# Kernel tuning notes

Hardware: AMD Instinct MI355X
Metric: run time of the kernel (lower is better)

## Reference

```python
import jax, jax.numpy as jnp
import numpy as np

FEATURE_DIM = 512


def setup_inputs() -> dict:
    key = jax.random.key(0)
    ks = jax.random.split(key, 12)
    B, Nv, Dv = 32, 1024, 768
    Nl, Dl = 77, 512
    D = FEATURE_DIM
    s = lambda fan_in: 1.0 / np.sqrt(fan_in)
    return {
        "fv": jax.random.normal(ks[0], (B, Nv, Dv), jnp.float32),
        "fl": jax.random.normal(ks[1], (B, Nl, Dl), jnp.float32),
        # linear_vk / linear_vv: Dv -> D (stored as [in, out])
        "W_vk": jax.random.uniform(ks[2], (Dv, D), jnp.float32, -s(Dv), s(Dv)),
        "b_vk": jax.random.uniform(ks[3], (D,), jnp.float32, -s(Dv), s(Dv)),
        "W_vv": jax.random.uniform(ks[4], (Dv, D), jnp.float32, -s(Dv), s(Dv)),
        "b_vv": jax.random.uniform(ks[5], (D,), jnp.float32, -s(Dv), s(Dv)),
        # linear_lk / linear_lv: Dl -> D
        "W_lk": jax.random.uniform(ks[6], (Dl, D), jnp.float32, -s(Dl), s(Dl)),
        "b_lk": jax.random.uniform(ks[7], (D,), jnp.float32, -s(Dl), s(Dl)),
        "W_lv": jax.random.uniform(ks[8], (Dl, D), jnp.float32, -s(Dl), s(Dl)),
        "b_lv": jax.random.uniform(ks[9], (D,), jnp.float32, -s(Dl), s(Dl)),
        # linear_m: nl(77) -> 768
        "W_m": jax.random.uniform(ks[10], (Nl, 768), jnp.float32, -s(Nl), s(Nl)),
        "b_m": jax.random.uniform(ks[11], (768,), jnp.float32, -s(Nl), s(Nl)),
    }


def reference(fv, fl, W_vk, b_vk, W_vv, b_vv, W_lk, b_lk, W_lv, b_lv, W_m, b_m):
    # projections
    fk_v = jnp.einsum("bvd,de->bve", fv, W_vk) + b_vk   # [B, Nv, D]
    fv_v = jnp.einsum("bvd,de->bve", fv, W_vv) + b_vv   # [B, Nv, D]
    fk_l = jnp.einsum("bld,de->ble", fl, W_lk) + b_lk   # [B, Nl, D]
    fv_l = jnp.einsum("bld,de->ble", fl, W_lv) + b_lv   # [B, Nl, D]
    # shared score matrix [B, Nl, Nv]
    a_raw = jnp.einsum("ble,bve->blv", fk_l, fk_v) / jnp.sqrt(
        jnp.asarray(FEATURE_DIM, fk_l.dtype))
    # dual softmax: over Nv for language queries, over Nl for vision queries
    fa_v = jnp.einsum("blv,bve->ble", jax.nn.softmax(a_raw, axis=-1), fv_v)  # [B, Nl, D]
    fa_l = jnp.einsum("bvl,ble->bve",
                      jax.nn.softmax(jnp.swapaxes(a_raw, -1, -2), axis=-1),
                      fv_l)                                                  # [B, Nv, D]
    # fm = fa_v @ fa_l^T -> [B, Nl, Nv]; transpose(1,2) -> [B, Nv, Nl]
    fm = jnp.einsum("bve,ble->bvl", fa_l, fa_v)          # [B, Nv, Nl]
    return jnp.einsum("bvl,lo->bvo", fm, W_m) + b_m      # [B, Nv, 768]
```

## Files before the change

### kernel.cpp

```cpp
#include <hip/hip_runtime.h>


using s16x8  = __attribute__((ext_vector_type(8))) short;
using f32x4v = __attribute__((ext_vector_type(4))) float;

__device__ __forceinline__ unsigned short f2bf(float f) {
  unsigned int u = __float_as_uint(f);
  u += 0x7fffu + ((u >> 16) & 1u);
  return (unsigned short)(u >> 16);
}
__device__ __forceinline__ float bf2f(unsigned short h) {
  return __uint_as_float(((unsigned int)h) << 16);
}
__device__ __forceinline__ void split2(float v, unsigned short &hh, unsigned short &ll) {
  hh = f2bf(v);
  ll = f2bf(v - bf2f(hh));
}
__device__ __forceinline__ void split8v(float4 a, float4 b, s16x8& H, s16x8& L) {
  unsigned short hh, ll;
  split2(a.x, hh, ll); H[0] = (short)hh; L[0] = (short)ll;
  split2(a.y, hh, ll); H[1] = (short)hh; L[1] = (short)ll;
  split2(a.z, hh, ll); H[2] = (short)hh; L[2] = (short)ll;
  split2(a.w, hh, ll); H[3] = (short)hh; L[3] = (short)ll;
  split2(b.x, hh, ll); H[4] = (short)hh; L[4] = (short)ll;
  split2(b.y, hh, ll); H[5] = (short)hh; L[5] = (short)ll;
  split2(b.z, hh, ll); H[6] = (short)hh; L[6] = (short)ll;
  split2(b.w, hh, ll); H[7] = (short)hh; L[7] = (short)ll;
}

__global__ __launch_bounds__(256) void prep_weight(const float* __restrict__ W,
                                                   unsigned short* __restrict__ Wh,
                                                   unsigned short* __restrict__ Wl,
                                                   int K, int N, int Kpad) {
  __shared__ float tile[32][33];
  int nb = blockIdx.x * 32, kb = blockIdx.y * 32;
  int tx = threadIdx.x & 31, ty = threadIdx.x >> 5;
  #pragma unroll
  for (int i = 0; i < 32; i += 8) {
    int k = kb + ty + i, n = nb + tx;
    tile[ty + i][tx] = (k < K && n < N) ? W[(long)k * N + n] : 0.f;
  }
  __syncthreads();
  #pragma unroll
  for (int i = 0; i < 32; i += 8) {
    int n = nb + ty + i, k = kb + tx;
    if (n < N && k < Kpad) {
      unsigned short hh, ll;
      split2(tile[tx][ty + i], hh, ll);
      Wh[(long)n * Kpad + k] = hh;
      Wl[(long)n * Kpad + k] = ll;
    }
  }
}

struct GemmArgs {
  const unsigned short *Ah, *Alo, *Bh, *Blo;
  const float *Af;
  int K;
  int Mld, Nld;
  int lda, ldb;
  long long sA, sB;
};

template <bool AF32, class Epi>
__global__ __launch_bounds__(256, 2) void gemm2(GemmArgs g, Epi epi) {
  __shared__ __align__(16) unsigned short sm[32768];

  const int t    = threadIdx.x;
  const int b    = blockIdx.z;
  const int m0   = blockIdx.y * 128;
  const int n0   = blockIdx.x * 128;
  const int lane = t & 63;
  const int w    = t >> 6;
  const int wr   = (w >> 1) * 64;
  const int wc   = (w & 1) * 64;

  const long long aBase = (long long)b * g.sA;
  const long long bBase = (long long)b * g.sB;

  const int rA0 = t >> 2, rA1 = 64 + (t >> 2), cc = t & 3;
  const int cOff = cc << 3;
  int mr0 = m0 + rA0; if (mr0 > g.Mld - 1) mr0 = g.Mld - 1;
  int mr1 = m0 + rA1; if (mr1 > g.Mld - 1) mr1 = g.Mld - 1;
  int nr0 = n0 + rA0; if (nr0 > g.Nld - 1) nr0 = g.Nld - 1;
  int nr1 = n0 + rA1; if (nr1 > g.Nld - 1) nr1 = g.Nld - 1;
  const long long aR0 = aBase + (long long)mr0 * g.lda;
  const long long aR1 = aBase + (long long)mr1 * g.lda;
  const long long bR0 = bBase + (long long)nr0 * g.ldb;
  const long long bR1 = bBase + (long long)nr1 * g.ldb;
  const int wA0 = rA0 * 32 + ((cc ^ ((rA0 >> 1) & 3)) << 3);
  const int wA1 = rA1 * 32 + ((cc ^ ((rA1 >> 1) & 3)) << 3);

  int roffA[4], roffB[4];
  #pragma unroll
  for (int i = 0; i < 4; ++i) {
    int row = wr + i * 16 + (lane & 15);
    int ch  = lane >> 4;
    roffA[i] = row * 32 + ((ch ^ ((row >> 1) & 3)) << 3);
    row = wc + i * 16 + (lane & 15);
    roffB[i] = row * 32 + ((ch ^ ((row >> 1) & 3)) << 3);
  }

  f32x4v acc[4][4];
  #pragma unroll
  for (int i = 0; i < 4; ++i)
    #pragma unroll
    for (int j = 0; j < 4; ++j)
      #pragma unroll
      for (int r = 0; r < 4; ++r) acc[i][j][r] = 0.f;

  float4 pa0, pa1, pa2, pa3;
  s16x8 pah0, pah1, pal0, pal1;
  s16x8 pbh0, pbh1, pbl0, pbl1;

  auto issueLoads = [&](int k0) {
    if constexpr (AF32) {
      const float* s0 = g.Af + (aR0 + k0 + cOff);
      const float* s1 = g.Af + (aR1 + k0 + cOff);
      pa0 = *(const float4*)s0; pa1 = *(const float4*)(s0 + 4);
      pa2 = *(const float4*)s1; pa3 = *(const float4*)(s1 + 4);
    } else {
      pah0 = *(const s16x8*)(g.Ah  + (aR0 + k0 + cOff));
      pah1 = *(const s16x8*)(g.Ah  + (aR1 + k0 + cOff));
      pal0 = *(const s16x8*)(g.Alo + (aR0 + k0 + cOff));
      pal1 = *(const s16x8*)(g.Alo + (aR1 + k0 + cOff));
    }
    pbh0 = *(const s16x8*)(g.Bh  + (bR0 + k0 + cOff));
    pbh1 = *(const s16x8*)(g.Bh  + (bR1 + k0 + cOff));
    pbl0 = *(const s16x8*)(g.Blo + (bR0 + k0 + cOff));
    pbl1 = *(const s16x8*)(g.Blo + (bR1 + k0 + cOff));
  };
  auto writeStage = [&](int p) {
    unsigned short* base = sm + p * 16384;
    if constexpr (AF32) {
      s16x8 H, L;
      split8v(pa0, pa1, H, L);
      *(s16x8*)(base + wA0) = H; *(s16x8*)(base + 4096 + wA0) = L;
      split8v(pa2, pa3, H, L);
      *(s16x8*)(base + wA1) = H; *(s16x8*)(base + 4096 + wA1) = L;
    } else {
      *(s16x8*)(base + wA0) = pah0; *(s16x8*)(base + wA1) = pah1;
      *(s16x8*)(base + 4096 + wA0) = pal0; *(s16x8*)(base + 4096 + wA1) = pal1;
    }
    *(s16x8*)(base + 8192  + wA0) = pbh0; *(s16x8*)(base + 8192  + wA1) = pbh1;
    *(s16x8*)(base + 12288 + wA0) = pbl0; *(s16x8*)(base + 12288 + wA1) = pbl1;
  };

  issueLoads(0);
  writeStage(0);
  int p = 0;
  const int nkt = g.K >> 5;
  for (int kt = 0; kt < nkt; ++kt) {
    __syncthreads();
    if (kt + 1 < nkt) issueLoads((kt + 1) << 5);
    unsigned short* base = sm + p * 16384;
    s16x8 ah[4], al[4], bh[4], bl[4];
    #pragma unroll
    for (int i = 0; i < 4; ++i) {
      ah[i] = *(const s16x8*)(base + roffA[i]);
      al[i] = *(const s16x8*)(base + 4096 + roffA[i]);
    }
    #pragma unroll
    for (int j = 0; j < 4; ++j) {
      bh[j] = *(const s16x8*)(base + 8192  + roffB[j]);
      bl[j] = *(const s16x8*)(base + 12288 + roffB[j]);
    }
    #pragma unroll
    for (int i = 0; i < 4; ++i)
      #pragma unroll
      for (int j = 0; j < 4; ++j) {
        acc[i][j] = __builtin_amdgcn_mfma_f32_16x16x32_bf16(ah[i], bh[j], acc[i][j], 0, 0, 0);
        acc[i][j] = __builtin_amdgcn_mfma_f32_16x16x32_bf16(ah[i], bl[j], acc[i][j], 0, 0, 0);
        acc[i][j] = __builtin_amdgcn_mfma_f32_16x16x32_bf16(al[i], bh[j], acc[i][j], 0, 0, 0);
      }
    if (kt + 1 < nkt) writeStage(p ^ 1);
    p ^= 1;
  }
  #pragma unroll
  for (int i = 0; i < 4; ++i)
    #pragma unroll
    for (int j = 0; j < 4; ++j) {
      int mm = m0 + wr + i * 16 + ((lane >> 4) << 2);
      int nn = n0 + wc + j * 16 + (lane & 15);
      epi(b, mm, nn, acc[i][j]);
    }
}

struct EpiBF16Pair {
  unsigned short *h, *lo; const float* bias; long long bs; int ld; int Mst;
  __device__ void operator()(int b, int m, int n, f32x4v v) const {
    float bb = bias ? bias[n] : 0.f;
    #pragma unroll
    for (int r = 0; r < 4; ++r) {
      int mm = m + r;
      if (mm < Mst) {
        long long o = (long long)b * bs + (long long)mm * ld + n;
        unsigned short hh, ll;
        split2(v[r] + bb, hh, ll);
        h[o] = hh; lo[o] = ll;
      }
    }
  }
};

struct EpiDualL {
  unsigned short *kh, *kl, *vh, *vl; const float *bk, *bv;
  __device__ void operator()(int, int m, int n, f32x4v v) const {
    bool lo512 = n < 512;
    float bb = lo512 ? bk[n] : bv[n - 512];
    int nn = lo512 ? n : n - 512;
    unsigned short* H = lo512 ? kh : vh;
    unsigned short* L = lo512 ? kl : vl;
    #pragma unroll
    for (int r = 0; r < 4; ++r) {
      int mm = m + r;
      if (mm < 2464) {
        long long o = (long long)mm * 512 + nn;
        unsigned short hh, ll;
        split2(v[r] + bb, hh, ll);
        H[o] = hh; L[o] = ll;
      }
    }
  }
};

struct EpiDualV {
  unsigned short *kh, *kl, *vh, *vl; const float *bk, *bv;
  __device__ void operator()(int, int m, int n, f32x4v v) const {
    if (n < 512) {
      float bb = bk[n];
      #pragma unroll
      for (int r = 0; r < 4; ++r) {
        long long o = (long long)(m + r) * 512 + n;
        unsigned short hh, ll;
        split2(v[r] + bb, hh, ll);
        kh[o] = hh; kl[o] = ll;
      }
    } else {
      int b2 = m >> 10, vv = m & 1023;
      float bb = bv[n - 512];
      ushort4 H, L;
      split2(v[0] + bb, H.x, L.x); split2(v[1] + bb, H.y, L.y);
      split2(v[2] + bb, H.z, L.z); split2(v[3] + bb, H.w, L.w);
      long long o = ((long long)b2 * 512 + (n - 512)) * 1024 + vv;
      *(ushort4*)(vh + o) = H;
      *(ushort4*)(vl + o) = L;
    }
  }
};

struct EpiScore {
  float* out;
  __device__ void operator()(int b, int m, int n, f32x4v v) const {
    #pragma unroll
    for (int r = 0; r < 4; ++r) {
      int mm = m + r;
      if (mm < 77)
        out[((long long)b * 77 + mm) * 1024 + n] = v[r] * 0.04419417382415922f;
    }
  }
};

struct EpiTransT {
  unsigned short *h, *lo;
  __device__ void operator()(int b, int m, int n, f32x4v v) const {
    #pragma unroll
    for (int r = 0; r < 4; ++r) {
      int mm = m + r;
      float val = (mm < 77) ? v[r] : 0.f;
      long long o = (long long)b * 98304 + (long long)n * 128 + mm;
      unsigned short hh, ll;
      split2(val, hh, ll);
      h[o] = hh; lo[o] = ll;
    }
  }
};

struct EpiOutB {
  float* out; const float* bias;
  __device__ void operator()(int b, int m, int n, f32x4v v) const {
    float bb = bias[n];
    #pragma unroll
    for (int r = 0; r < 4; ++r)
      out[(long long)(b * 1024 + m + r) * 768 + n] = v[r] + bb;
  }
};

__global__ __launch_bounds__(256) void softmax_rows(const float* __restrict__ a,
                                                    unsigned short* __restrict__ Ph,
                                                    unsigned short* __restrict__ Plo) {
  long row = blockIdx.x;
  const float* src = a + row * 1024;
  int t = threadIdx.x;
  float4 x = ((const float4*)src)[t];
  float mx = fmaxf(fmaxf(x.x, x.y), fmaxf(x.z, x.w));
  #pragma unroll
  for (int o = 32; o; o >>= 1) mx = fmaxf(mx, __shfl_xor(mx, o));
  __shared__ float red[4], red2[4];
  int w = t >> 6;
  if ((t & 63) == 0) red[w] = mx;
  __syncthreads();
  mx = fmaxf(fmaxf(red[0], red[1]), fmaxf(red[2], red[3]));
  float e0 = __expf(x.x - mx), e1 = __expf(x.y - mx);
  float e2 = __expf(x.z - mx), e3 = __expf(x.w - mx);
  float s = e0 + e1 + e2 + e3;
  #pragma unroll
  for (int o = 32; o; o >>= 1) s += __shfl_xor(s, o);
  if ((t & 63) == 0) red2[w] = s;
  __syncthreads();
  s = red2[0] + red2[1] + red2[2] + red2[3];
  float inv = 1.f / s;
  ushort4 H, L;
  split2(e0 * inv, H.x, L.x); split2(e1 * inv, H.y, L.y);
  split2(e2 * inv, H.z, L.z); split2(e3 * inv, H.w, L.w);
  long o = row * 1024 + (long)t * 4;
  *(ushort4*)(Ph + o)  = H;
  *(ushort4*)(Plo + o) = L;
}

__global__ __launch_bounds__(128) void softmax_cols(const float* __restrict__ a,
                                                    unsigned short* __restrict__ Ph,
                                                    unsigned short* __restrict__ Plo) {
  __shared__ float tile[77 * 129];
  __shared__ float inv[128];
  int t = threadIdx.x;
  int c = blockIdx.x;
  int b = blockIdx.y;
  const float* src = a + (long)b * 77 * 1024 + c * 128;
  for (int r = 0; r < 77; ++r) tile[r * 129 + t] = src[(long)r * 1024 + t];
  __syncthreads();
  float mx = -1e30f;
  for (int r = 0; r < 77; ++r) mx = fmaxf(mx, tile[r * 129 + t]);
  float s = 0.f;
  for (int r = 0; r < 77; ++r) {
    float e = __expf(tile[r * 129 + t] - mx);
    tile[r * 129 + t] = e;
    s += e;
  }
  inv[t] = 1.f / s;
  __syncthreads();
  unsigned short* dh = Ph  + ((long)b * 1024 + c * 128) * 128;
  unsigned short* dl = Plo + ((long)b * 1024 + c * 128) * 128;
  for (int vb = 0; vb < 128; vb += 2) {
    int v = vb + (t >> 6);
    int k = (t & 63) * 2;
    float iv = inv[v];
    float p0 = (k     < 77) ? tile[k * 129 + v] * iv       : 0.f;
    float p1 = (k + 1 < 77) ? tile[(k + 1) * 129 + v] * iv : 0.f;
    ushort2 H, L;
    split2(p0, H.x, L.x); split2(p1, H.y, L.y);
    *(ushort2*)(dh + (long)v * 128 + k) = H;
    *(ushort2*)(dl + (long)v * 128 + k) = L;
  }
}

extern "C" void kernel_launch(void* const* d_in, const int* in_sizes, int n_in,
                              void* d_out, int out_size, void* d_ws, size_t ws_size,
                              hipStream_t stream) {
  const float* fv   = (const float*)d_in[0];
  const float* fl   = (const float*)d_in[1];
  const float* W_vk = (const float*)d_in[2];
  const float* b_vk = (const float*)d_in[3];
  const float* W_vv = (const float*)d_in[4];
  const float* b_vv = (const float*)d_in[5];
  const float* W_lk = (const float*)d_in[6];
  const float* b_lk = (const float*)d_in[7];
  const float* W_lv = (const float*)d_in[8];
  const float* b_lv = (const float*)d_in[9];
  const float* W_m  = (const float*)d_in[10];
  const float* b_m  = (const float*)d_in[11];

  char* base = (char*)d_ws;
  size_t off = 0;
  auto take = [&](size_t bytes) -> char* {
    char* p = base + off;
    off = (off + bytes + 255) & ~(size_t)255;
    return p;
  };

  unsigned short* wcatv_h = (unsigned short*)take(1572864);
  unsigned short* wcatv_l = (unsigned short*)take(1572864);
  unsigned short* wcatl_h = (unsigned short*)take(1048576);
  unsigned short* wcatl_l = (unsigned short*)take(1048576);
  unsigned short* wm_h    = (unsigned short*)take(196608);
  unsigned short* wm_l    = (unsigned short*)take(196608);
  unsigned short* fkl_h  = (unsigned short*)take(2523136);
  unsigned short* fkl_l  = (unsigned short*)take(2523136);
  unsigned short* fvl_h  = (unsigned short*)take(2523136);
  unsigned short* fvl_l  = (unsigned short*)take(2523136);
  unsigned short* fkv_h  = (unsigned short*)take(33554432);
  unsigned short* fkv_l  = (unsigned short*)take(33554432);
  unsigned short* fvvT_h = (unsigned short*)take(33554432);
  unsigned short* fvvT_l = (unsigned short*)take(33554432);
  float*          araw   = (float*)take(10092544);
  unsigned short* p1_h   = (unsigned short*)take(5046272);
  unsigned short* p1_l   = (unsigned short*)take(5046272);
  unsigned short* p2t_h  = (unsigned short*)take(8388608);
  unsigned short* p2t_l  = (unsigned short*)take(8388608);
  unsigned short* fav_h  = (unsigned short*)take(4194304);
  unsigned short* fav_l  = (unsigned short*)take(4194304);
  unsigned short* s_h    = (unsigned short*)take(1048576);
  unsigned short* s_l    = (unsigned short*)take(1048576);
  unsigned short* tt_h   = (unsigned short*)take(6291456);
  unsigned short* tt_l   = (unsigned short*)take(6291456);

  if (off > ws_size) return;

  prep_weight<<<dim3(16, 24), 256, 0, stream>>>(W_vk, wcatv_h, wcatv_l, 768, 512, 768);
  prep_weight<<<dim3(16, 24), 256, 0, stream>>>(W_vv, wcatv_h + 512 * 768, wcatv_l + 512 * 768, 768, 512, 768);
  prep_weight<<<dim3(16, 16), 256, 0, stream>>>(W_lk, wcatl_h, wcatl_l, 512, 512, 512);
  prep_weight<<<dim3(16, 16), 256, 0, stream>>>(W_lv, wcatl_h + 512 * 512, wcatl_l + 512 * 512, 512, 512, 512);
  prep_weight<<<dim3(24, 4), 256, 0, stream>>>(W_m, wm_h, wm_l, 77, 768, 128);

  {
    GemmArgs g{}; g.Af = fl; g.Bh = wcatl_h; g.Blo = wcatl_l;
    g.K = 512; g.Mld = 2464; g.Nld = 1024; g.lda = 512; g.ldb = 512; g.sA = 0; g.sB = 0;
    EpiDualL e{fkl_h, fkl_l, fvl_h, fvl_l, b_lk, b_lv};
    gemm2<true, EpiDualL><<<dim3(8, 20, 1), 256, 0, stream>>>(g, e);
  }
  {
    GemmArgs g{}; g.Af = fv; g.Bh = wcatv_h; g.Blo = wcatv_l;
    g.K = 768; g.Mld = 32768; g.Nld = 1024; g.lda = 768; g.ldb = 768; g.sA = 0; g.sB = 0;
    EpiDualV e{fkv_h, fkv_l, fvvT_h, fvvT_l, b_vk, b_vv};
    gemm2<true, EpiDualV><<<dim3(8, 256, 1), 256, 0, stream>>>(g, e);
  }
  {
    GemmArgs g{}; g.Ah = fkl_h; g.Alo = fkl_l; g.Bh = fkv_h; g.Blo = fkv_l;
    g.K = 512; g.Mld = 77; g.Nld = 1024; g.lda = 512; g.ldb = 512;
    g.sA = 77 * 512; g.sB = 1024 * 512;
    EpiScore e{araw};
    gemm2<false, EpiScore><<<dim3(8, 1, 32), 256, 0, stream>>>(g, e);
  }
  softmax_rows<<<2464, 256, 0, stream>>>(araw, p1_h, p1_l);
  softmax_cols<<<dim3(8, 32), 128, 0, stream>>>(araw, p2t_h, p2t_l);
  {
    GemmArgs g{}; g.Ah = p1_h; g.Alo = p1_l; g.Bh = fvvT_h; g.Blo = fvvT_l;
    g.K = 1024; g.Mld = 77; g.Nld = 512; g.lda = 1024; g.ldb = 1024;
    g.sA = 77 * 1024; g.sB = 512 * 1024;
    EpiBF16Pair e{fav_h, fav_l, nullptr, 128 * 512, 512, 128};
    gemm2<false, EpiBF16Pair><<<dim3(4, 1, 32), 256, 0, stream>>>(g, e);
  }
  {
    GemmArgs g{}; g.Ah = fvl_h; g.Alo = fvl_l; g.Bh = fav_h; g.Blo = fav_l;
    g.K = 512; g.Mld = 77; g.Nld = 128; g.lda = 512; g.ldb = 512;
    g.sA = 77 * 512; g.sB = 128 * 512;
    EpiBF16Pair e{s_h, s_l, nullptr, 128 * 128, 128, 128};
    gemm2<false, EpiBF16Pair><<<dim3(1, 1, 32), 256, 0, stream>>>(g, e);
  }
  {
    GemmArgs g{}; g.Ah = s_h; g.Alo = s_l; g.Bh = wm_h; g.Blo = wm_l;
    g.K = 128; g.Mld = 128; g.Nld = 768; g.lda = 128; g.ldb = 128;
    g.sA = 128 * 128; g.sB = 0;
    EpiTransT e{tt_h, tt_l};
    gemm2<false, EpiTransT><<<dim3(6, 1, 32), 256, 0, stream>>>(g, e);
  }
  {
    GemmArgs g{}; g.Ah = p2t_h; g.Alo = p2t_l; g.Bh = tt_h; g.Blo = tt_l;
    g.K = 128; g.Mld = 1024; g.Nld = 768; g.lda = 128; g.ldb = 128;
    g.sA = 1024 * 128; g.sB = 768 * 128;
    EpiOutB e{(float*)d_out, b_m};
    gemm2<false, EpiOutB><<<dim3(6, 8, 32), 256, 0, stream>>>(g, e);
  }
  (void)in_sizes; (void)n_in; (void)out_size;
}
```

Measured before the change: 591.0 us.

## Load bf16 GEMM operands directly into LDS and swizzle workgroup order

Bf16 operand tiles now go from global memory straight into shared memory through global_load_lds, with no register staging and no separate LDS write step. The fp32 A path keeps its register split. The big vision projection GEMM also remaps workgroup IDs into an XCD-aware order to improve L2 locality. The cost is a full vmcnt(0) wait before each barrier, which may serialise the prefetch with compute, and the DMA destination layout must match the swizzled layout the fragment reads expect.

```diff
diff --git a/kernel.cpp b/kernel.cpp
--- a/kernel.cpp
+++ b/kernel.cpp
@@ -28,6 +28,13 @@
   split2(b.w, hh, ll); H[7] = (short)hh; L[7] = (short)ll;
 }
 
+__device__ __forceinline__ void gload16(const unsigned short* g, unsigned short* l) {
+  __builtin_amdgcn_global_load_lds(
+      (const __attribute__((address_space(1))) unsigned int*)(const void*)g,
+      (__attribute__((address_space(3))) unsigned int*)(void*)l,
+      16, 0, 0);
+}
+
 __global__ __launch_bounds__(256) void prep_weight(const float* __restrict__ W,
                                                    unsigned short* __restrict__ Wh,
                                                    unsigned short* __restrict__ Wl,
@@ -62,14 +69,23 @@
   long long sA, sB;
 };
 
-template <bool AF32, class Epi>
+template <bool AF32, bool SWZ, class Epi>
 __global__ __launch_bounds__(256, 2) void gemm2(GemmArgs g, Epi epi) {
   __shared__ __align__(16) unsigned short sm[32768];
 
+  int bidx = blockIdx.x, bidy = blockIdx.y;
+  if constexpr (SWZ) {
+    int nx = gridDim.x;
+    int nwg = nx * gridDim.y;
+    int orig = bidx + bidy * nx;
+    int swz = (orig & 7) * (nwg >> 3) + (orig >> 3);
+    bidx = swz % nx; bidy = swz / nx;
+  }
+
   const int t    = threadIdx.x;
   const int b    = blockIdx.z;
-  const int m0   = blockIdx.y * 128;
-  const int n0   = blockIdx.x * 128;
+  const int m0   = bidy * 128;
+  const int n0   = bidx * 128;
   const int lane = t & 63;
   const int w    = t >> 6;
   const int wr   = (w >> 1) * 64;
@@ -78,16 +94,26 @@
   const long long aBase = (long long)b * g.sA;
   const long long bBase = (long long)b * g.sB;
 
+  const int rw  = (w << 5) + (lane >> 2);
+  const int cl  = lane & 3;
+  const int sck = ((cl ^ ((rw >> 1) & 3)) << 3);
+  int br0 = n0 + rw;      if (br0 > g.Nld - 1) br0 = g.Nld - 1;
+  int br1 = n0 + rw + 16; if (br1 > g.Nld - 1) br1 = g.Nld - 1;
+  const long long bR0d = bBase + (long long)br0 * g.ldb + sck;
+  const long long bR1d = bBase + (long long)br1 * g.ldb + sck;
+  int ar0 = m0 + rw;      if (ar0 > g.Mld - 1) ar0 = g.Mld - 1;
+  int ar1 = m0 + rw + 16; if (ar1 > g.Mld - 1) ar1 = g.Mld - 1;
+  const long long aR0d = aBase + (long long)ar0 * g.lda + sck;
+  const long long aR1d = aBase + (long long)ar1 * g.lda + sck;
+  const int dQ0 = w * 1024;
+  const int dQ1 = w * 1024 + 512;
+
   const int rA0 = t >> 2, rA1 = 64 + (t >> 2), cc = t & 3;
   const int cOff = cc << 3;
   int mr0 = m0 + rA0; if (mr0 > g.Mld - 1) mr0 = g.Mld - 1;
   int mr1 = m0 + rA1; if (mr1 > g.Mld - 1) mr1 = g.Mld - 1;
-  int nr0 = n0 + rA0; if (nr0 > g.Nld - 1) nr0 = g.Nld - 1;
-  int nr1 = n0 + rA1; if (nr1 > g.Nld - 1) nr1 = g.Nld - 1;
   const long long aR0 = aBase + (long long)mr0 * g.lda;
   const long long aR1 = aBase + (long long)mr1 * g.lda;
-  const long long bR0 = bBase + (long long)nr0 * g.ldb;
-  const long long bR1 = bBase + (long long)nr1 * g.ldb;
   const int wA0 = rA0 * 32 + ((cc ^ ((rA0 >> 1) & 3)) << 3);
   const int wA1 = rA1 * 32 + ((cc ^ ((rA1 >> 1) & 3)) << 3);
 
@@ -110,49 +136,51 @@
       for (int r = 0; r < 4; ++r) acc[i][j][r] = 0.f;
 
   float4 pa0, pa1, pa2, pa3;
-  s16x8 pah0, pah1, pal0, pal1;
-  s16x8 pbh0, pbh1, pbl0, pbl1;
-
-  auto issueLoads = [&](int k0) {
+
+  auto issueDMA = [&](int k0, int p) {
+    unsigned short* bb = sm + p * 16384;
+    gload16(g.Bh  + (bR0d + k0), bb + 8192  + dQ0);
+    gload16(g.Bh  + (bR1d + k0), bb + 8192  + dQ1);
+    gload16(g.Blo + (bR0d + k0), bb + 12288 + dQ0);
+    gload16(g.Blo + (bR1d + k0), bb + 12288 + dQ1);
+    if constexpr (!AF32) {
+      gload16(g.Ah  + (aR0d + k0), bb + dQ0);
+      gload16(g.Ah  + (aR1d + k0), bb + dQ1);
+      gload16(g.Alo + (aR0d + k0), bb + 4096 + dQ0);
+      gload16(g.Alo + (aR1d + k0), bb + 4096 + dQ1);
+    }
+  };
+  auto issueLoadsA = [&](int k0) {
     if constexpr (AF32) {
       const float* s0 = g.Af + (aR0 + k0 + cOff);
       const float* s1 = g.Af + (aR1 + k0 + cOff);
       pa0 = *(const float4*)s0; pa1 = *(const float4*)(s0 + 4);
       pa2 = *(const float4*)s1; pa3 = *(const float4*)(s1 + 4);
-    } else {
-      pah0 = *(const s16x8*)(g.Ah  + (aR0 + k0 + cOff));
-      pah1 = *(const s16x8*)(g.Ah  + (aR1 + k0 + cOff));
-      pal0 = *(const s16x8*)(g.Alo + (aR0 + k0 + cOff));
-      pal1 = *(const s16x8*)(g.Alo + (aR1 + k0 + cOff));
-    }
-    pbh0 = *(const s16x8*)(g.Bh  + (bR0 + k0 + cOff));
-    pbh1 = *(const s16x8*)(g.Bh  + (bR1 + k0 + cOff));
-    pbl0 = *(const s16x8*)(g.Blo + (bR0 + k0 + cOff));
-    pbl1 = *(const s16x8*)(g.Blo + (bR1 + k0 + cOff));
+    }
   };
-  auto writeStage = [&](int p) {
-    unsigned short* base = sm + p * 16384;
+  auto writeStageA = [&](int p) {
     if constexpr (AF32) {
+      unsigned short* base = sm + p * 16384;
       s16x8 H, L;
       split8v(pa0, pa1, H, L);
       *(s16x8*)(base + wA0) = H; *(s16x8*)(base + 4096 + wA0) = L;
       split8v(pa2, pa3, H, L);
       *(s16x8*)(base + wA1) = H; *(s16x8*)(base + 4096 + wA1) = L;
-    } else {
-      *(s16x8*)(base + wA0) = pah0; *(s16x8*)(base + wA1) = pah1;
-      *(s16x8*)(base + 4096 + wA0) = pal0; *(s16x8*)(base + 4096 + wA1) = pal1;
-    }
-    *(s16x8*)(base + 8192  + wA0) = pbh0; *(s16x8*)(base + 8192  + wA1) = pbh1;
-    *(s16x8*)(base + 12288 + wA0) = pbl0; *(s16x8*)(base + 12288 + wA1) = pbl1;
+    }
   };
 
-  issueLoads(0);
-  writeStage(0);
+  issueDMA(0, 0);
+  issueLoadsA(0);
+  writeStageA(0);
   int p = 0;
   const int nkt = g.K >> 5;
   for (int kt = 0; kt < nkt; ++kt) {
+    asm volatile("s_waitcnt vmcnt(0)" ::: "memory");
     __syncthreads();
-    if (kt + 1 < nkt) issueLoads((kt + 1) << 5);
+    if (kt + 1 < nkt) {
+      issueDMA((kt + 1) << 5, p ^ 1);
+      issueLoadsA((kt + 1) << 5);
+    }
     unsigned short* base = sm + p * 16384;
     s16x8 ah[4], al[4], bh[4], bl[4];
     #pragma unroll
@@ -173,7 +201,7 @@
         acc[i][j] = __builtin_amdgcn_mfma_f32_16x16x32_bf16(ah[i], bl[j], acc[i][j], 0, 0, 0);
         acc[i][j] = __builtin_amdgcn_mfma_f32_16x16x32_bf16(al[i], bh[j], acc[i][j], 0, 0, 0);
       }
-    if (kt + 1 < nkt) writeStage(p ^ 1);
+    if (kt + 1 < nkt) writeStageA(p ^ 1);
     p ^= 1;
   }
   #pragma unroll
@@ -416,20 +444,20 @@
     GemmArgs g{}; g.Af = fl; g.Bh = wcatl_h; g.Blo = wcatl_l;
     g.K = 512; g.Mld = 2464; g.Nld = 1024; g.lda = 512; g.ldb = 512; g.sA = 0; g.sB = 0;
     EpiDualL e{fkl_h, fkl_l, fvl_h, fvl_l, b_lk, b_lv};
-    gemm2<true, EpiDualL><<<dim3(8, 20, 1), 256, 0, stream>>>(g, e);
+    gemm2<true, false, EpiDualL><<<dim3(8, 20, 1), 256, 0, stream>>>(g, e);
   }
   {
     GemmArgs g{}; g.Af = fv; g.Bh = wcatv_h; g.Blo = wcatv_l;
     g.K = 768; g.Mld = 32768; g.Nld = 1024; g.lda = 768; g.ldb = 768; g.sA = 0; g.sB = 0;
     EpiDualV e{fkv_h, fkv_l, fvvT_h, fvvT_l, b_vk, b_vv};
-    gemm2<true, EpiDualV><<<dim3(8, 256, 1), 256, 0, stream>>>(g, e);
+    gemm2<true, true, EpiDualV><<<dim3(8, 256, 1), 256, 0, stream>>>(g, e);
   }
   {
     GemmArgs g{}; g.Ah = fkl_h; g.Alo = fkl_l; g.Bh = fkv_h; g.Blo = fkv_l;
     g.K = 512; g.Mld = 77; g.Nld = 1024; g.lda = 512; g.ldb = 512;
     g.sA = 77 * 512; g.sB = 1024 * 512;
     EpiScore e{araw};
-    gemm2<false, EpiScore><<<dim3(8, 1, 32), 256, 0, stream>>>(g, e);
+    gemm2<false, false, EpiScore><<<dim3(8, 1, 32), 256, 0, stream>>>(g, e);
   }
   softmax_rows<<<2464, 256, 0, stream>>>(araw, p1_h, p1_l);
   softmax_cols<<<dim3(8, 32), 128, 0, stream>>>(araw, p2t_h, p2t_l);
@@ -438,28 +466,28 @@
     g.K = 1024; g.Mld = 77; g.Nld = 512; g.lda = 1024; g.ldb = 1024;
     g.sA = 77 * 1024; g.sB = 512 * 1024;
     EpiBF16Pair e{fav_h, fav_l, nullptr, 128 * 512, 512, 128};
-    gemm2<false, EpiBF16Pair><<<dim3(4, 1, 32), 256, 0, stream>>>(g, e);
+    gemm2<false, false, EpiBF16Pair><<<dim3(4, 1, 32), 256, 0, stream>>>(g, e);
   }
   {
     GemmArgs g{}; g.Ah = fvl_h; g.Alo = fvl_l; g.Bh = fav_h; g.Blo = fav_l;
     g.K = 512; g.Mld = 77; g.Nld = 128; g.lda = 512; g.ldb = 512;
     g.sA = 77 * 512; g.sB = 128 * 512;
     EpiBF16Pair e{s_h, s_l, nullptr, 128 * 128, 128, 128};
-    gemm2<false, EpiBF16Pair><<<dim3(1, 1, 32), 256, 0, stream>>>(g, e);
+    gemm2<false, false, EpiBF16Pair><<<dim3(1, 1, 32), 256, 0, stream>>>(g, e);
   }
   {
     GemmArgs g{}; g.Ah = s_h; g.Alo = s_l; g.Bh = wm_h; g.Blo = wm_l;
     g.K = 128; g.Mld = 128; g.Nld = 768; g.lda = 128; g.ldb = 128;
     g.sA = 128 * 128; g.sB = 0;
     EpiTransT e{tt_h, tt_l};
-    gemm2<false, EpiTransT><<<dim3(6, 1, 32), 256, 0, stream>>>(g, e);
+    gemm2<false, false, EpiTransT><<<dim3(6, 1, 32), 256, 0, stream>>>(g, e);
   }
   {
     GemmArgs g{}; g.Ah = p2t_h; g.Alo = p2t_l; g.Bh = tt_h; g.Blo = tt_l;
     g.K = 128; g.Mld = 1024; g.Nld = 768; g.lda = 128; g.ldb = 128;
     g.sA = 1024 * 128; g.sB = 768 * 128;
     EpiOutB e{(float*)d_out, b_m};
-    gemm2<false, EpiOutB><<<dim3(6, 8, 32), 256, 0, stream>>>(g, e);
+    gemm2<false, false, EpiOutB><<<dim3(6, 8, 32), 256, 0, stream>>>(g, e);
   }
   (void)in_sizes; (void)n_in; (void)out_size;
 }
```

Result: no change. 585.7 us (-0.9%).
